# Kernel optimization log

Measured on AMD Instinct MI355X. Metric: run time of the kernel, lower is better.

Reference implementation:

```python
import jax, jax.numpy as jnp
import numpy as np

E = 128
H = 4
D = E // H  # 32


def setup_inputs() -> dict:
    key = jax.random.key(0)
    ks = jax.random.split(key, 5)
    b, n = 4, 4096
    x = jax.random.normal(ks[0], (b, n, E), dtype=jnp.float32)
    # Linear weights stored as [in, out] (i.e. torch weight transposed)
    W_qkv = jax.random.normal(ks[1], (E, 3 * E), dtype=jnp.float32) * (1.0 / np.sqrt(E))
    b_qkv = jax.random.normal(ks[2], (3 * E,), dtype=jnp.float32) * 0.01
    W_proj = jax.random.normal(ks[3], (E, E), dtype=jnp.float32) * (1.0 / np.sqrt(E))
    b_proj = jax.random.normal(ks[4], (E,), dtype=jnp.float32) * 0.01
    return {"x": x, "W_qkv": W_qkv, "b_qkv": b_qkv, "W_proj": W_proj, "b_proj": b_proj}


def reference(x, W_qkv, b_qkv, W_proj, b_proj):
    b, n, e = x.shape
    # qkv projection; last dim layout is (h d qkv) with qkv innermost,
    # matching rearrange('b n (h d qkv) -> qkv b h n d')
    qkv = (x @ W_qkv + b_qkv).reshape(b, n, H, D, 3)
    qkv = jnp.transpose(qkv, (4, 0, 2, 1, 3))  # [3, b, h, n, d]
    q, k, v = qkv[0], qkv[1], qkv[2]
    # NOTE: original scales by sqrt(e) (=sqrt(128)), not sqrt(d). Faithful.
    scale = 1.0 / np.float32(np.sqrt(e))
    scores = jnp.einsum('bhnd,bhmd->bhnm', q, k) * scale  # [b,h,n,n]
    att = jax.nn.softmax(scores, axis=-1)
    # dropout is identity in eval mode (reference baseline)
    out = jnp.einsum('bhnm,bhmd->bhnd', att, v)  # [b,h,n,d]
    out = jnp.transpose(out, (0, 2, 1, 3)).reshape(b, n, e)  # b n (h d)
    return out @ W_proj + b_proj
```

## Files before the change

### kernel.cpp

```cpp
#include <hip/hip_runtime.h>
#include <stdint.h>

#define N_SEQ 4096
#define MFMA16 __builtin_amdgcn_mfma_f32_16x16x32_bf16

typedef float f32x4 __attribute__((ext_vector_type(4)));
typedef float f32x2 __attribute__((ext_vector_type(2)));
typedef unsigned short u16x8 __attribute__((ext_vector_type(8)));
typedef unsigned short u16x4 __attribute__((ext_vector_type(4)));
typedef unsigned int u32x2 __attribute__((ext_vector_type(2)));
typedef __bf16 bf16x8 __attribute__((ext_vector_type(8)));

static __device__ __forceinline__ float bf2f(unsigned short u) {
    unsigned v = ((unsigned)u) << 16;
    return __builtin_bit_cast(float, v);
}

__global__ __launch_bounds__(256) void wrepack_kernel(
    const float* __restrict__ Wq, unsigned short* __restrict__ WqF)
{
    int idx = blockIdx.x * 256 + threadIdx.x;
    int i = idx & 7, l = (idx >> 3) & 63, fr = idx >> 9;
    int ct = fr >> 2, ks = fr & 3;
    int k = ks * 32 + (l >> 4) * 8 + i;
    int col = ct * 16 + (l & 15);
    WqF[idx] = __builtin_bit_cast(unsigned short, (__bf16)Wq[k * 384 + col]);
}

__global__ __launch_bounds__(256) void wrepack2_kernel(
    const float* __restrict__ Wp, unsigned short* __restrict__ WpF)
{
    int idx = blockIdx.x * 256 + threadIdx.x;
    int i = idx & 7, l = (idx >> 3) & 63, fr = idx >> 9;
    int ct = fr >> 2, ks = fr & 3;
    int k = ks * 32 + (l >> 4) * 8 + i;
    int col = ct * 16 + (l & 15);
    WpF[idx] = __builtin_bit_cast(unsigned short, (__bf16)Wp[k * 128 + col]);
}

__global__ __launch_bounds__(256) void qkv_kernel(
    const float* __restrict__ x, const unsigned short* __restrict__ WqF,
    const float* __restrict__ bq, unsigned short* __restrict__ Qo,
    unsigned short* __restrict__ KFo, unsigned short* __restrict__ VFo)
{
    const int tid = threadIdx.x, lane = tid & 63, w = tid >> 6;
    const int g = lane >> 4, lo = lane & 15;
    const long r0 = (long)blockIdx.x * 32;
    const float SL = (float)(0.08838834764831845 * 1.4426950408889634);
    const f32x4 zf = {0.f, 0.f, 0.f, 0.f};

    bf16x8 xf[2][4];
    #pragma unroll
    for (int rt = 0; rt < 2; ++rt) {
        const float* xr = x + (r0 + rt * 16 + lo) * 128 + g * 8;
        #pragma unroll
        for (int ks = 0; ks < 4; ++ks) {
            f32x4 a = *(const f32x4*)&xr[ks * 32];
            f32x4 b = *(const f32x4*)&xr[ks * 32 + 4];
            bf16x8 f;
            f[0] = (__bf16)a[0]; f[1] = (__bf16)a[1]; f[2] = (__bf16)a[2]; f[3] = (__bf16)a[3];
            f[4] = (__bf16)b[0]; f[5] = (__bf16)b[1]; f[6] = (__bf16)b[2]; f[7] = (__bf16)b[3];
            xf[rt][ks] = f;
        }
    }
    f32x4 acc[2][6];
    #pragma unroll
    for (int rt = 0; rt < 2; ++rt)
        #pragma unroll
        for (int c = 0; c < 6; ++c) acc[rt][c] = zf;

    const u16x8* wp = (const u16x8*)WqF + (size_t)(w * 24) * 64 + lane;
    #pragma unroll
    for (int c = 0; c < 6; ++c)
        #pragma unroll
        for (int ks = 0; ks < 4; ++ks) {
            bf16x8 wf = __builtin_bit_cast(bf16x8, wp[(c * 4 + ks) * 64]);
            acc[0][c] = MFMA16(xf[0][ks], wf, acc[0][c], 0, 0, 0);
            acc[1][c] = MFMA16(xf[1][ks], wf, acc[1][c], 0, 0, 0);
        }

    const int bb = (int)(r0 >> 12), nn0 = (int)(r0 & 4095);
    const int bh = bb * 4 + w;
    const int t = nn0 >> 6, kvb = nn0 & 63;
    const int kk = kvb >> 5;
    #pragma unroll
    for (int c = 0; c < 6; ++c) {
        int col = (w * 6 + c) * 16 + lo;
        int rem = col - w * 96;
        int d = rem / 3, s = rem % 3;
        float bias = bq[col];
        #pragma unroll
        for (int rt = 0; rt < 2; ++rt) {
            float scale = (s == 0) ? SL : 1.0f;
            unsigned short bits[4];
            #pragma unroll
            for (int j = 0; j < 4; ++j)
                bits[j] = __builtin_bit_cast(unsigned short,
                              (__bf16)((acc[rt][c][j] + bias) * scale));
            if (s == 0) {
                long base = ((long)bh * 4096 + nn0 + rt * 16 + 4 * g) * 32 + d;
                #pragma unroll
                for (int j = 0; j < 4; ++j) Qo[base + (long)j * 32] = bits[j];
            } else if (s == 1) {
                int ct_k = (kvb >> 4) + rt;
                long base = (long)((bh * 64 + t) * 4 + ct_k) * 512
                          + ((d >> 3) * 16 + 4 * g) * 8 + (d & 7);
                #pragma unroll
                for (int j = 0; j < 4; ++j) KFo[base + j * 8] = bits[j];
            } else {
                int lg = rt * 2 + (g >> 1);
                long base = (long)(((bh * 64 + t) * 2 + kk) * 2 + (d >> 4)) * 512
                          + (lg * 16 + (d & 15)) * 8 + ((4 * g) & 7);
                u16x4 pk = {bits[0], bits[1], bits[2], bits[3]};
                *(u16x4*)&VFo[base] = pk;
            }
        }
    }
}

__global__ __launch_bounds__(256, 4) void attn_kernel(
    const unsigned short* __restrict__ Q, const unsigned short* __restrict__ KF,
    const unsigned short* __restrict__ VF, unsigned short* __restrict__ AO)
{
    __shared__ __align__(16) unsigned char smem[16384];

    const int tid = threadIdx.x, lane = tid & 63, w = tid >> 6;
    const int g = lane >> 4, lo = lane & 15;
    const int wq = w & 1, wh = w >> 1;

    const int bid = blockIdx.x;
    const int vid = (bid & 7) * 128 + (bid >> 3);
    const int qi = vid & 63, bh = vid >> 6;
    const int q0 = qi * 64 + wq * 32;

    bf16x8 qf[2];
    #pragma unroll
    for (int rt = 0; rt < 2; ++rt) {
        const unsigned short* p = Q + ((long)bh * 4096 + q0 + rt * 16 + lo) * 32 + g * 8;
        qf[rt] = __builtin_bit_cast(bf16x8, *(const u16x8*)p);
    }
    bf16x8 onesf;
    {
        u16x8 ou = {0x3F80,0x3F80,0x3F80,0x3F80,0x3F80,0x3F80,0x3F80,0x3F80};
        onesf = __builtin_bit_cast(bf16x8, ou);
    }
    const f32x4 zf = {0.f, 0.f, 0.f, 0.f};
    f32x4 o_[2][2] = {{zf, zf}, {zf, zf}};
    f32x4 ls[2]    = {zf, zf};

    int woff[2][4], roff[2][2];
    #pragma unroll
    for (int qt = 0; qt < 2; ++qt) {
        int q = lo + 16 * qt;
        #pragma unroll
        for (int ct = 0; ct < 4; ++ct) {
            int kvb = 16 * ct + 4 * g;
            woff[qt][ct] = q * 64 + (((kvb >> 3) ^ (q & 7)) * 8) + ((kvb >> 2) & 1) * 4;
        }
    }
    #pragma unroll
    for (int rt = 0; rt < 2; ++rt) {
        int q = lo + 16 * rt;
        #pragma unroll
        for (int kk = 0; kk < 2; ++kk)
            roff[rt][kk] = q * 64 + ((((4 * kk) + g) ^ (q & 7)) * 8);
    }
    unsigned short* B = (unsigned short*)(smem + w * 4096);

    const u16x8* kp = (const u16x8*)KF + ((long)bh * 64 + wh * 32) * 256 + lane;
    const u16x8* vp = (const u16x8*)VF + ((long)bh * 64 + wh * 32) * 256 + lane;

    u16x8 K0[4], K1[4], Vb[4];
    #pragma unroll
    for (int i = 0; i < 4; ++i) K0[i] = kp[i * 64];
    kp += 256;

#define PACK2(S_, CT_)                                                          \
    do {                                                                        \
        unsigned a0 = __builtin_bit_cast(unsigned, __builtin_amdgcn_exp2f(S_[0][CT_][0]));\
        unsigned a1 = __builtin_bit_cast(unsigned, __builtin_amdgcn_exp2f(S_[0][CT_][1]));\
        unsigned a2 = __builtin_bit_cast(unsigned, __builtin_amdgcn_exp2f(S_[0][CT_][2]));\
        unsigned a3 = __builtin_bit_cast(unsigned, __builtin_amdgcn_exp2f(S_[0][CT_][3]));\
        u32x2 w0_;                                                              \
        w0_[0] = __builtin_amdgcn_perm(a1, a0, 0x07060302u);                    \
        w0_[1] = __builtin_amdgcn_perm(a3, a2, 0x07060302u);                    \
        *(u16x4*)&B[woff[0][CT_]] = __builtin_bit_cast(u16x4, w0_);             \
        unsigned c0 = __builtin_bit_cast(unsigned, __builtin_amdgcn_exp2f(S_[1][CT_][0]));\
        unsigned c1 = __builtin_bit_cast(unsigned, __builtin_amdgcn_exp2f(S_[1][CT_][1]));\
        unsigned c2 = __builtin_bit_cast(unsigned, __builtin_amdgcn_exp2f(S_[1][CT_][2]));\
        unsigned c3 = __builtin_bit_cast(unsigned, __builtin_amdgcn_exp2f(S_[1][CT_][3]));\
        u32x2 w1_;                                                              \
        w1_[0] = __builtin_amdgcn_perm(c1, c0, 0x07060302u);                    \
        w1_[1] = __builtin_amdgcn_perm(c3, c2, 0x07060302u);                    \
        *(u16x4*)&B[woff[1][CT_]] = __builtin_bit_cast(u16x4, w1_);             \
    } while (0)

#define PV(KK_)                                                                 \
    do {                                                                        \
        __builtin_amdgcn_s_setprio(1);                                          \
        _Pragma("unroll")                                                       \
        for (int rt = 0; rt < 2; ++rt) {                                        \
            bf16x8 paf = __builtin_bit_cast(bf16x8,                             \
                *(const u16x8*)&B[roff[rt][KK_]]);                              \
            ls[rt] = MFMA16(paf, onesf, ls[rt], 0, 0, 0);                       \
            o_[rt][0] = MFMA16(paf, __builtin_bit_cast(bf16x8, Vb[KK_*2+0]),    \
                               o_[rt][0], 0, 0, 0);                             \
            o_[rt][1] = MFMA16(paf, __builtin_bit_cast(bf16x8, Vb[KK_*2+1]),    \
                               o_[rt][1], 0, 0, 0);                             \
        }                                                                       \
        __builtin_amdgcn_s_setprio(0);                                          \
    } while (0)

#define BODY(KC, KN) do {                                                      \
    _Pragma("unroll")                                                          \
    for (int i = 0; i < 4; ++i) KN[i] = kp[i * 64];                            \
    kp += 256;                                                                 \
    _Pragma("unroll")                                                          \
    for (int i = 0; i < 4; ++i) Vb[i] = vp[i * 64];                            \
    vp += 256;                                                                 \
    f32x4 s_[2][4];                                                            \
    __builtin_amdgcn_s_setprio(1);                                             \
    _Pragma("unroll")                                                          \
    for (int ct = 0; ct < 4; ++ct) {                                           \
        bf16x8 kfr = __builtin_bit_cast(bf16x8, KC[ct]);                       \
        s_[0][ct] = MFMA16(kfr, qf[0], zf, 0, 0, 0);                           \
        s_[1][ct] = MFMA16(kfr, qf[1], zf, 0, 0, 0);                           \
    }                                                                          \
    __builtin_amdgcn_s_setprio(0);                                             \
    PACK2(s_, 0);                                                              \
    PACK2(s_, 1);                                                              \
    __builtin_amdgcn_sched_barrier(0);                                         \
    PV(0);                                                                     \
    PACK2(s_, 2);                                                              \
    PACK2(s_, 3);                                                              \
    __builtin_amdgcn_sched_barrier(0);                                         \
    PV(1);                                                                     \
    __builtin_amdgcn_sched_barrier(0);                                         \
} while (0)

    #pragma unroll 1
    for (int t = 0; t < 32; t += 2) {
        BODY(K0, K1);
        BODY(K1, K0);
    }
#undef BODY
#undef PV
#undef PACK2

    __syncthreads();
    float* sc = (float*)smem;
    float* myp = sc + (wq * 64 + lane) * 24;
    if (wh == 1) {
        #pragma unroll
        for (int rt = 0; rt < 2; ++rt)
            #pragma unroll
            for (int dt = 0; dt < 2; ++dt)
                *(f32x4*)&myp[(rt * 2 + dt) * 4] = o_[rt][dt];
        *(f32x4*)&myp[16] = ls[0];
        *(f32x4*)&myp[20] = ls[1];
    }
    __syncthreads();
    if (wh == 0) {
        #pragma unroll
        for (int rt = 0; rt < 2; ++rt) {
            #pragma unroll
            for (int dt = 0; dt < 2; ++dt)
                o_[rt][dt] += *(const f32x4*)&myp[(rt * 2 + dt) * 4];
            ls[rt] += *(const f32x4*)&myp[16 + rt * 4];
        }
        const int bb = bh >> 2, h = bh & 3;
        #pragma unroll
        for (int rt = 0; rt < 2; ++rt)
            #pragma unroll
            for (int j = 0; j < 4; ++j) {
                float rl = __builtin_amdgcn_rcpf(ls[rt][j]);
                int row = q0 + rt * 16 + 4 * g + j;
                #pragma unroll
                for (int dt = 0; dt < 2; ++dt) {
                    int e = h * 32 + lo + 16 * dt;
                    float val = o_[rt][dt][j] * rl;
                    AO[((long)bb * N_SEQ + row) * 128 + e] =
                        __builtin_bit_cast(unsigned short, (__bf16)val);
                }
            }
    }
}

__global__ __launch_bounds__(256) void proj_kernel(
    const unsigned short* __restrict__ AO, const unsigned short* __restrict__ WpF,
    const float* __restrict__ bp, float* __restrict__ out)
{
    const int tid = threadIdx.x, lane = tid & 63, w = tid >> 6;
    const int g = lane >> 4, lo = lane & 15;
    const long r0 = (long)blockIdx.x * 32;
    const f32x4 zf = {0.f, 0.f, 0.f, 0.f};

    bf16x8 xf[2][4];
    #pragma unroll
    for (int rt = 0; rt < 2; ++rt) {
        const unsigned short* xr = AO + (r0 + rt * 16 + lo) * 128 + g * 8;
        #pragma unroll
        for (int ks = 0; ks < 4; ++ks)
            xf[rt][ks] = __builtin_bit_cast(bf16x8, *(const u16x8*)&xr[ks * 32]);
    }
    f32x4 acc[2][2] = {{zf, zf}, {zf, zf}};

    const u16x8* wp = (const u16x8*)WpF + (size_t)(w * 8) * 64 + lane;
    #pragma unroll
    for (int c = 0; c < 2; ++c)
        #pragma unroll
        for (int ks = 0; ks < 4; ++ks) {
            bf16x8 wf = __builtin_bit_cast(bf16x8, wp[(c * 4 + ks) * 64]);
            acc[0][c] = MFMA16(xf[0][ks], wf, acc[0][c], 0, 0, 0);
            acc[1][c] = MFMA16(xf[1][ks], wf, acc[1][c], 0, 0, 0);
        }

    #pragma unroll
    for (int c = 0; c < 2; ++c) {
        int col = (w * 2 + c) * 16 + lo;
        float bias = bp[col];
        #pragma unroll
        for (int rt = 0; rt < 2; ++rt) {
            long base = (r0 + rt * 16 + 4 * g) * 128 + col;
            #pragma unroll
            for (int j = 0; j < 4; ++j)
                out[base + (long)j * 128] = acc[rt][c][j] + bias;
        }
    }
}

extern "C" void kernel_launch(void* const* d_in, const int* in_sizes, int n_in,
                              void* d_out, int out_size, void* d_ws, size_t ws_size,
                              hipStream_t stream)
{
    const float* x  = (const float*)d_in[0];
    const float* Wq = (const float*)d_in[1];
    const float* bq = (const float*)d_in[2];
    const float* Wp = (const float*)d_in[3];
    const float* bp = (const float*)d_in[4];
    float* out = (float*)d_out;

    unsigned short* Qw   = (unsigned short*)d_ws;
    unsigned short* KFw  = Qw   + (size_t)16 * 4096 * 32;
    unsigned short* VFw  = KFw  + (size_t)16 * 4096 * 32;
    unsigned short* AOw  = VFw  + (size_t)16 * 4096 * 32;
    unsigned short* WqFw = AOw  + (size_t)16 * 4096 * 32;
    unsigned short* WpFw = WqFw + (size_t)49152;

    wrepack_kernel<<<192, 256, 0, stream>>>(Wq, WqFw);
    wrepack2_kernel<<<64, 256, 0, stream>>>(Wp, WpFw);
    qkv_kernel<<<512, 256, 0, stream>>>(x, WqFw, bq, Qw, KFw, VFw);
    attn_kernel<<<1024, 256, 0, stream>>>(Qw, KFw, VFw, AOw);
    proj_kernel<<<512, 256, 0, stream>>>(AOw, WpFw, bp, out);
}
```

Measured before the change: 81.80 us.

## Merge weight repack kernels, halve GEMM row tiles, double-buffer V in attention

The two weight-repack kernels become one launch, which removes a kernel launch. The qkv and proj GEMM kernels now handle 16 rows per block instead of 32, doubling the grid to 1024 blocks to raise parallelism on the small projections. The attention loop now double-buffers V registers the same way K is handled, prefetching the next V tile one iteration ahead to hide global load latency. This costs extra registers in attn_kernel under launch_bounds(256,4), and the smaller GEMM tiles reuse each loaded weight fragment less.

```diff
diff --git a/kernel.cpp b/kernel.cpp
--- a/kernel.cpp
+++ b/kernel.cpp
@@ -17,25 +17,24 @@
 }
 
 __global__ __launch_bounds__(256) void wrepack_kernel(
-    const float* __restrict__ Wq, unsigned short* __restrict__ WqF)
+    const float* __restrict__ Wq, const float* __restrict__ Wp,
+    unsigned short* __restrict__ WqF, unsigned short* __restrict__ WpF)
 {
     int idx = blockIdx.x * 256 + threadIdx.x;
-    int i = idx & 7, l = (idx >> 3) & 63, fr = idx >> 9;
-    int ct = fr >> 2, ks = fr & 3;
-    int k = ks * 32 + (l >> 4) * 8 + i;
-    int col = ct * 16 + (l & 15);
-    WqF[idx] = __builtin_bit_cast(unsigned short, (__bf16)Wq[k * 384 + col]);
-}
-
-__global__ __launch_bounds__(256) void wrepack2_kernel(
-    const float* __restrict__ Wp, unsigned short* __restrict__ WpF)
-{
-    int idx = blockIdx.x * 256 + threadIdx.x;
-    int i = idx & 7, l = (idx >> 3) & 63, fr = idx >> 9;
-    int ct = fr >> 2, ks = fr & 3;
-    int k = ks * 32 + (l >> 4) * 8 + i;
-    int col = ct * 16 + (l & 15);
-    WpF[idx] = __builtin_bit_cast(unsigned short, (__bf16)Wp[k * 128 + col]);
+    if (idx < 49152) {
+        int i = idx & 7, l = (idx >> 3) & 63, fr = idx >> 9;
+        int ct = fr >> 2, ks = fr & 3;
+        int k = ks * 32 + (l >> 4) * 8 + i;
+        int col = ct * 16 + (l & 15);
+        WqF[idx] = __builtin_bit_cast(unsigned short, (__bf16)Wq[k * 384 + col]);
+    } else {
+        int j = idx - 49152;
+        int i = j & 7, l = (j >> 3) & 63, fr = j >> 9;
+        int ct = fr >> 2, ks = fr & 3;
+        int k = ks * 32 + (l >> 4) * 8 + i;
+        int col = ct * 16 + (l & 15);
+        WpF[j] = __builtin_bit_cast(unsigned short, (__bf16)Wp[k * 128 + col]);
+    }
 }
 
 __global__ __launch_bounds__(256) void qkv_kernel(
@@ -45,14 +44,13 @@
 {
     const int tid = threadIdx.x, lane = tid & 63, w = tid >> 6;
     const int g = lane >> 4, lo = lane & 15;
-    const long r0 = (long)blockIdx.x * 32;
+    const long r0 = (long)blockIdx.x * 16;
     const float SL = (float)(0.08838834764831845 * 1.4426950408889634);
     const f32x4 zf = {0.f, 0.f, 0.f, 0.f};
 
-    bf16x8 xf[2][4];
-    #pragma unroll
-    for (int rt = 0; rt < 2; ++rt) {
-        const float* xr = x + (r0 + rt * 16 + lo) * 128 + g * 8;
+    bf16x8 xf[4];
+    {
+        const float* xr = x + (r0 + lo) * 128 + g * 8;
         #pragma unroll
         for (int ks = 0; ks < 4; ++ks) {
             f32x4 a = *(const f32x4*)&xr[ks * 32];
@@ -60,14 +58,12 @@
             bf16x8 f;
             f[0] = (__bf16)a[0]; f[1] = (__bf16)a[1]; f[2] = (__bf16)a[2]; f[3] = (__bf16)a[3];
             f[4] = (__bf16)b[0]; f[5] = (__bf16)b[1]; f[6] = (__bf16)b[2]; f[7] = (__bf16)b[3];
-            xf[rt][ks] = f;
-        }
-    }
-    f32x4 acc[2][6];
-    #pragma unroll
-    for (int rt = 0; rt < 2; ++rt)
-        #pragma unroll
-        for (int c = 0; c < 6; ++c) acc[rt][c] = zf;
+            xf[ks] = f;
+        }
+    }
+    f32x4 acc[6];
+    #pragma unroll
+    for (int c = 0; c < 6; ++c) acc[c] = zf;
 
     const u16x8* wp = (const u16x8*)WqF + (size_t)(w * 24) * 64 + lane;
     #pragma unroll
@@ -75,8 +71,7 @@
         #pragma unroll
         for (int ks = 0; ks < 4; ++ks) {
             bf16x8 wf = __builtin_bit_cast(bf16x8, wp[(c * 4 + ks) * 64]);
-            acc[0][c] = MFMA16(xf[0][ks], wf, acc[0][c], 0, 0, 0);
-            acc[1][c] = MFMA16(xf[1][ks], wf, acc[1][c], 0, 0, 0);
+            acc[c] = MFMA16(xf[ks], wf, acc[c], 0, 0, 0);
         }
 
     const int bb = (int)(r0 >> 12), nn0 = (int)(r0 & 4095);
@@ -89,31 +84,28 @@
         int rem = col - w * 96;
         int d = rem / 3, s = rem % 3;
         float bias = bq[col];
-        #pragma unroll
-        for (int rt = 0; rt < 2; ++rt) {
-            float scale = (s == 0) ? SL : 1.0f;
-            unsigned short bits[4];
-            #pragma unroll
-            for (int j = 0; j < 4; ++j)
-                bits[j] = __builtin_bit_cast(unsigned short,
-                              (__bf16)((acc[rt][c][j] + bias) * scale));
-            if (s == 0) {
-                long base = ((long)bh * 4096 + nn0 + rt * 16 + 4 * g) * 32 + d;
-                #pragma unroll
-                for (int j = 0; j < 4; ++j) Qo[base + (long)j * 32] = bits[j];
-            } else if (s == 1) {
-                int ct_k = (kvb >> 4) + rt;
-                long base = (long)((bh * 64 + t) * 4 + ct_k) * 512
-                          + ((d >> 3) * 16 + 4 * g) * 8 + (d & 7);
-                #pragma unroll
-                for (int j = 0; j < 4; ++j) KFo[base + j * 8] = bits[j];
-            } else {
-                int lg = rt * 2 + (g >> 1);
-                long base = (long)(((bh * 64 + t) * 2 + kk) * 2 + (d >> 4)) * 512
-                          + (lg * 16 + (d & 15)) * 8 + ((4 * g) & 7);
-                u16x4 pk = {bits[0], bits[1], bits[2], bits[3]};
-                *(u16x4*)&VFo[base] = pk;
-            }
+        float scale = (s == 0) ? SL : 1.0f;
+        unsigned short bits[4];
+        #pragma unroll
+        for (int j = 0; j < 4; ++j)
+            bits[j] = __builtin_bit_cast(unsigned short,
+                          (__bf16)((acc[c][j] + bias) * scale));
+        if (s == 0) {
+            long base = ((long)bh * 4096 + nn0 + 4 * g) * 32 + d;
+            #pragma unroll
+            for (int j = 0; j < 4; ++j) Qo[base + (long)j * 32] = bits[j];
+        } else if (s == 1) {
+            int ct_k = (kvb >> 4) & 3;
+            long base = (long)((bh * 64 + t) * 4 + ct_k) * 512
+                      + ((d >> 3) * 16 + 4 * g) * 8 + (d & 7);
+            #pragma unroll
+            for (int j = 0; j < 4; ++j) KFo[base + j * 8] = bits[j];
+        } else {
+            int lg = ((kvb >> 3) & 3) | (g >> 1);
+            long base = (long)(((bh * 64 + t) * 2 + kk) * 2 + (d >> 4)) * 512
+                      + (lg * 16 + (d & 15)) * 8 + ((4 * g) & 7);
+            u16x4 pk = {bits[0], bits[1], bits[2], bits[3]};
+            *(u16x4*)&VFo[base] = pk;
         }
     }
 }
@@ -170,10 +162,10 @@
     const u16x8* kp = (const u16x8*)KF + ((long)bh * 64 + wh * 32) * 256 + lane;
     const u16x8* vp = (const u16x8*)VF + ((long)bh * 64 + wh * 32) * 256 + lane;
 
-    u16x8 K0[4], K1[4], Vb[4];
-    #pragma unroll
-    for (int i = 0; i < 4; ++i) K0[i] = kp[i * 64];
-    kp += 256;
+    u16x8 K0[4], K1[4], V0[4], V1[4];
+    #pragma unroll
+    for (int i = 0; i < 4; ++i) { K0[i] = kp[i * 64]; V0[i] = vp[i * 64]; }
+    kp += 256; vp += 256;
 
 #define PACK2(S_, CT_)                                                          \
     do {                                                                        \
@@ -195,7 +187,7 @@
         *(u16x4*)&B[woff[1][CT_]] = __builtin_bit_cast(u16x4, w1_);             \
     } while (0)
 
-#define PV(KK_)                                                                 \
+#define PV(KK_, VC)                                                             \
     do {                                                                        \
         __builtin_amdgcn_s_setprio(1);                                          \
         _Pragma("unroll")                                                       \
@@ -203,20 +195,20 @@
             bf16x8 paf = __builtin_bit_cast(bf16x8,                             \
                 *(const u16x8*)&B[roff[rt][KK_]]);                              \
             ls[rt] = MFMA16(paf, onesf, ls[rt], 0, 0, 0);                       \
-            o_[rt][0] = MFMA16(paf, __builtin_bit_cast(bf16x8, Vb[KK_*2+0]),    \
+            o_[rt][0] = MFMA16(paf, __builtin_bit_cast(bf16x8, VC[KK_*2+0]),    \
                                o_[rt][0], 0, 0, 0);                             \
-            o_[rt][1] = MFMA16(paf, __builtin_bit_cast(bf16x8, Vb[KK_*2+1]),    \
+            o_[rt][1] = MFMA16(paf, __builtin_bit_cast(bf16x8, VC[KK_*2+1]),    \
                                o_[rt][1], 0, 0, 0);                             \
         }                                                                       \
         __builtin_amdgcn_s_setprio(0);                                          \
     } while (0)
 
-#define BODY(KC, KN) do {                                                      \
+#define BODY(KC, KN, VC, VN) do {                                              \
     _Pragma("unroll")                                                          \
     for (int i = 0; i < 4; ++i) KN[i] = kp[i * 64];                            \
     kp += 256;                                                                 \
     _Pragma("unroll")                                                          \
-    for (int i = 0; i < 4; ++i) Vb[i] = vp[i * 64];                            \
+    for (int i = 0; i < 4; ++i) VN[i] = vp[i * 64];                            \
     vp += 256;                                                                 \
     f32x4 s_[2][4];                                                            \
     __builtin_amdgcn_s_setprio(1);                                             \
@@ -230,18 +222,18 @@
     PACK2(s_, 0);                                                              \
     PACK2(s_, 1);                                                              \
     __builtin_amdgcn_sched_barrier(0);                                         \
-    PV(0);                                                                     \
+    PV(0, VC);                                                                 \
     PACK2(s_, 2);                                                              \
     PACK2(s_, 3);                                                              \
     __builtin_amdgcn_sched_barrier(0);                                         \
-    PV(1);                                                                     \
+    PV(1, VC);                                                                 \
     __builtin_amdgcn_sched_barrier(0);                                         \
 } while (0)
 
     #pragma unroll 1
     for (int t = 0; t < 32; t += 2) {
-        BODY(K0, K1);
-        BODY(K1, K0);
+        BODY(K0, K1, V0, V1);
+        BODY(K1, K0, V1, V0);
     }
 #undef BODY
 #undef PV
@@ -292,18 +284,17 @@
 {
     const int tid = threadIdx.x, lane = tid & 63, w = tid >> 6;
     const int g = lane >> 4, lo = lane & 15;
-    const long r0 = (long)blockIdx.x * 32;
+    const long r0 = (long)blockIdx.x * 16;
     const f32x4 zf = {0.f, 0.f, 0.f, 0.f};
 
-    bf16x8 xf[2][4];
-    #pragma unroll
-    for (int rt = 0; rt < 2; ++rt) {
-        const unsigned short* xr = AO + (r0 + rt * 16 + lo) * 128 + g * 8;
+    bf16x8 xf[4];
+    {
+        const unsigned short* xr = AO + (r0 + lo) * 128 + g * 8;
         #pragma unroll
         for (int ks = 0; ks < 4; ++ks)
-            xf[rt][ks] = __builtin_bit_cast(bf16x8, *(const u16x8*)&xr[ks * 32]);
-    }
-    f32x4 acc[2][2] = {{zf, zf}, {zf, zf}};
+            xf[ks] = __builtin_bit_cast(bf16x8, *(const u16x8*)&xr[ks * 32]);
+    }
+    f32x4 acc[2] = {zf, zf};
 
     const u16x8* wp = (const u16x8*)WpF + (size_t)(w * 8) * 64 + lane;
     #pragma unroll
@@ -311,21 +302,17 @@
         #pragma unroll
         for (int ks = 0; ks < 4; ++ks) {
             bf16x8 wf = __builtin_bit_cast(bf16x8, wp[(c * 4 + ks) * 64]);
-            acc[0][c] = MFMA16(xf[0][ks], wf, acc[0][c], 0, 0, 0);
-            acc[1][c] = MFMA16(xf[1][ks], wf, acc[1][c], 0, 0, 0);
+            acc[c] = MFMA16(xf[ks], wf, acc[c], 0, 0, 0);
         }
 
     #pragma unroll
     for (int c = 0; c < 2; ++c) {
         int col = (w * 2 + c) * 16 + lo;
         float bias = bp[col];
-        #pragma unroll
-        for (int rt = 0; rt < 2; ++rt) {
-            long base = (r0 + rt * 16 + 4 * g) * 128 + col;
-            #pragma unroll
-            for (int j = 0; j < 4; ++j)
-                out[base + (long)j * 128] = acc[rt][c][j] + bias;
-        }
+        long base = (r0 + 4 * g) * 128 + col;
+        #pragma unroll
+        for (int j = 0; j < 4; ++j)
+            out[base + (long)j * 128] = acc[c][j] + bias;
     }
 }
 
@@ -347,9 +334,8 @@
     unsigned short* WqFw = AOw  + (size_t)16 * 4096 * 32;
     unsigned short* WpFw = WqFw + (size_t)49152;
 
-    wrepack_kernel<<<192, 256, 0, stream>>>(Wq, WqFw);
-    wrepack2_kernel<<<64, 256, 0, stream>>>(Wp, WpFw);
-    qkv_kernel<<<512, 256, 0, stream>>>(x, WqFw, bq, Qw, KFw, VFw);
+    wrepack_kernel<<<256, 256, 0, stream>>>(Wq, Wp, WqFw, WpFw);
+    qkv_kernel<<<1024, 256, 0, stream>>>(x, WqFw, bq, Qw, KFw, VFw);
     attn_kernel<<<1024, 256, 0, stream>>>(Qw, KFw, VFw, AOw);
-    proj_kernel<<<512, 256, 0, stream>>>(AOw, WpFw, bp, out);
-}
+    proj_kernel<<<1024, 256, 0, stream>>>(AOw, WpFw, bp, out);
+}
```

Measured after the change: 89.41 us. 1.09x slower.
